# Optimization experiments

Measured on AMD Instinct MI355X. Metric: run time of the kernel, lower is better.

Reference implementation:

```python
import jax, jax.numpy as jnp
import numpy as np

N = 1024
X_DIM = 128
Y_DIM = 128
HIDDEN = 256


def setup_inputs() -> dict:
    key = jax.random.key(0)
    ks = jax.random.split(key, 6)
    x_samples = jax.random.normal(ks[0], (N, X_DIM), dtype=jnp.float32)
    y_samples = jax.random.normal(ks[1], (N, Y_DIM), dtype=jnp.float32)
    in_dim = X_DIM + Y_DIM
    # Linear params (kaiming-uniform-ish small init)
    W1 = jax.random.normal(ks[2], (in_dim, HIDDEN), dtype=jnp.float32) / np.sqrt(in_dim)
    b1 = jnp.zeros((HIDDEN,), dtype=jnp.float32)
    W2 = jax.random.normal(ks[3], (HIDDEN, 1), dtype=jnp.float32) / np.sqrt(HIDDEN)
    b2 = jnp.zeros((1,), dtype=jnp.float32)
    return {"x_samples": x_samples, "y_samples": y_samples,
            "W1": W1, "b1": b1, "W2": W2, "b2": b2}


def reference(x_samples, y_samples, W1, b1, W2, b2):
    n = y_samples.shape[0]
    W1x, W1y = W1[:X_DIM], W1[X_DIM:]
    xp = x_samples @ W1x          # [N, H]  (x_tile[i, j] = x[j])
    yp = y_samples @ W1y          # [N, H]  (y_tile[i, j] = y[i])
    # T0: F(cat([x_i, y_i])) on the diagonal pairs -> [N, 1]
    T0 = jax.nn.relu(xp + yp + b1) @ W2 + b2
    # T1: F over all pairs (i, j) -> [N, N, 1]
    h = jax.nn.relu(yp[:, None, :] + xp[None, :, :] + b1)   # [N, N, H]
    T1 = h @ W2 + b2                                        # [N, N, 1]
    lse = jax.scipy.special.logsumexp(T1, axis=1)           # [N, 1] over dim=1
    lower_bound = T0.mean() - (lse.mean() - jnp.log(jnp.float32(n)))
    return lower_bound
```

## Files before the change

### kernel.cpp

```cpp
#include <hip/hip_runtime.h>

#define N_SAMP 1024
#define XD     128
#define HID    256


__global__ __launch_bounds__(256) void gemm_xy(
    const float* __restrict__ x, const float* __restrict__ y,
    const float* __restrict__ W1, const float* __restrict__ b1,
    float* __restrict__ xpb, float* __restrict__ yp)
{
    const int k  = threadIdx.x;
    const int r0 = blockIdx.x * 4;

    float ax0 = 0.f, ax1 = 0.f, ax2 = 0.f, ax3 = 0.f;
    float ay0 = 0.f, ay1 = 0.f, ay2 = 0.f, ay3 = 0.f;

    #pragma unroll 4
    for (int d = 0; d < XD; ++d) {
        const float wx = W1[d * HID + k];
        const float wy = W1[(XD + d) * HID + k];
        ax0 = fmaf(x[(r0 + 0) * XD + d], wx, ax0);
        ax1 = fmaf(x[(r0 + 1) * XD + d], wx, ax1);
        ax2 = fmaf(x[(r0 + 2) * XD + d], wx, ax2);
        ax3 = fmaf(x[(r0 + 3) * XD + d], wx, ax3);
        ay0 = fmaf(y[(r0 + 0) * XD + d], wy, ay0);
        ay1 = fmaf(y[(r0 + 1) * XD + d], wy, ay1);
        ay2 = fmaf(y[(r0 + 2) * XD + d], wy, ay2);
        ay3 = fmaf(y[(r0 + 3) * XD + d], wy, ay3);
    }

    const float bk = b1[k];
    xpb[(r0 + 0) * HID + k] = ax0 + bk;
    xpb[(r0 + 1) * HID + k] = ax1 + bk;
    xpb[(r0 + 2) * HID + k] = ax2 + bk;
    xpb[(r0 + 3) * HID + k] = ax3 + bk;
    yp [(r0 + 0) * HID + k] = ay0;
    yp [(r0 + 1) * HID + k] = ay1;
    yp [(r0 + 2) * HID + k] = ay2;
    yp [(r0 + 3) * HID + k] = ay3;
}

__global__ __launch_bounds__(256) void pair_lse(
    const float* __restrict__ yp, const float* __restrict__ xpb,
    const float* __restrict__ W2,
    float* __restrict__ S, float* __restrict__ T0sum)
{
    const int STRIDE = 260;
    __shared__ float ys[16 * 260];
    __shared__ float xs[16 * 260];

    const int tid = threadIdx.x;
    const int bi  = blockIdx.y;
    const int bj  = blockIdx.x;

    for (int idx = tid * 4; idx < 16 * 256; idx += 1024) {
        const int r = idx >> 8, c = idx & 255;
        *(float4*)&ys[r * STRIDE + c] = *(const float4*)&yp [(bi * 16 + r) * HID + c];
        *(float4*)&xs[r * STRIDE + c] = *(const float4*)&xpb[(bj * 16 + r) * HID + c];
    }
    __syncthreads();

    const int ti = tid >> 4;
    const int tj = tid & 15;
    const float* yrow = &ys[ti * STRIDE];
    const float* xrow = &xs[tj * STRIDE];

    float acc = 0.f;
    #pragma unroll 8
    for (int c = 0; c < HID; c += 4) {
        const float4 a = *(const float4*)&yrow[c];
        const float4 b = *(const float4*)&xrow[c];
        const float4 w = *(const float4*)&W2[c];
        acc = fmaf(fmaxf(a.x + b.x, 0.f), w.x, acc);
        acc = fmaf(fmaxf(a.y + b.y, 0.f), w.y, acc);
        acc = fmaf(fmaxf(a.z + b.z, 0.f), w.z, acc);
        acc = fmaf(fmaxf(a.w + b.w, 0.f), w.w, acc);
    }

    float e = __expf(acc);
    #pragma unroll
    for (int off = 8; off; off >>= 1) e += __shfl_xor(e, off, 16);
    const int gi = bi * 16 + ti;
    if (tj == 0) atomicAdd(&S[gi], e);

    if (bi == bj) {
        float dv = (ti == tj) ? acc : 0.f;
        #pragma unroll
        for (int off = 32; off; off >>= 1) dv += __shfl_xor(dv, off, 64);
        if ((tid & 63) == 0) atomicAdd(T0sum, dv);
    }
}

__global__ __launch_bounds__(256) void finalize(
    const float* __restrict__ S, const float* __restrict__ T0sum,
    const float* __restrict__ b2, float* __restrict__ out)
{
    __shared__ float red[4];
    const int tid = threadIdx.x;

    float ls = 0.f;
    for (int i = tid; i < N_SAMP; i += 256) ls += logf(S[i]);
    #pragma unroll
    for (int off = 32; off; off >>= 1) ls += __shfl_xor(ls, off, 64);
    if ((tid & 63) == 0) red[tid >> 6] = ls;
    __syncthreads();

    if (tid == 0) {
        const float lse_sum = red[0] + red[1] + red[2] + red[3];
        const float t0_mean  = T0sum[0] / (float)N_SAMP + b2[0];
        const float lse_mean = lse_sum / (float)N_SAMP + b2[0] - logf((float)N_SAMP);
        out[0] = t0_mean - lse_mean;
    }
}

extern "C" void kernel_launch(void* const* d_in, const int* in_sizes, int n_in,
                              void* d_out, int out_size, void* d_ws, size_t ws_size,
                              hipStream_t stream)
{
    const float* x  = (const float*)d_in[0];
    const float* y  = (const float*)d_in[1];
    const float* W1 = (const float*)d_in[2];
    const float* b1 = (const float*)d_in[3];
    const float* W2 = (const float*)d_in[4];
    const float* b2 = (const float*)d_in[5];

    float* ws   = (float*)d_ws;
    float* S    = ws;
    float* T0s  = ws + 1024;
    float* xpb  = ws + 2048;
    float* yp   = ws + 2048 + N_SAMP * HID;

    hipMemsetAsync(d_ws, 0, (1024 + 1) * sizeof(float), stream);

    gemm_xy <<<dim3(N_SAMP / 4), dim3(256), 0, stream>>>(x, y, W1, b1, xpb, yp);
    pair_lse<<<dim3(64, 64),     dim3(256), 0, stream>>>(yp, xpb, W2, S, T0s);
    finalize<<<dim3(1),          dim3(256), 0, stream>>>(S, T0s, b2, (float*)d_out);
}
```

Measured before the change: 118.2 us.

## Register-tile pair_lse: 8 y-rows per wave with wave-uniform loads, 64 x-rows in LDS

Restructures the pairwise kernel so each thread computes 8 (i,j) pairs. The y rows are wave-uniform and read straight from global memory, which should turn them into scalar or broadcast loads, while a 64-row x tile is staged in LDS. This cuts the LDS reads per FMA and the number of blocks and atomics, and reuses each x element across 8 y rows. In exchange it uses more registers and has fewer blocks (512), which may limit occupancy, and the per-lane LDS row reads with stride 260 could hit bank conflicts.

Result: no change. 119.1 us (+0.7%).

```diff
diff --git a/kernel.cpp b/kernel.cpp
--- a/kernel.cpp
+++ b/kernel.cpp
@@ -41,54 +41,72 @@
     yp [(r0 + 3) * HID + k] = ay3;
 }
 
-__global__ __launch_bounds__(256) void pair_lse(
+#define XSTR 260
+__global__ __launch_bounds__(256, 2) void pair_lse(
     const float* __restrict__ yp, const float* __restrict__ xpb,
     const float* __restrict__ W2,
     float* __restrict__ S, float* __restrict__ T0sum)
 {
-    const int STRIDE = 260;
-    __shared__ float ys[16 * 260];
-    __shared__ float xs[16 * 260];
+    __shared__ float xs[64 * XSTR];
 
     const int tid = threadIdx.x;
+    const int bj  = blockIdx.x;
     const int bi  = blockIdx.y;
-    const int bj  = blockIdx.x;
 
-    for (int idx = tid * 4; idx < 16 * 256; idx += 1024) {
+    for (int idx = tid * 4; idx < 64 * 256; idx += 1024) {
         const int r = idx >> 8, c = idx & 255;
-        *(float4*)&ys[r * STRIDE + c] = *(const float4*)&yp [(bi * 16 + r) * HID + c];
-        *(float4*)&xs[r * STRIDE + c] = *(const float4*)&xpb[(bj * 16 + r) * HID + c];
+        *(float4*)&xs[r * XSTR + c] = *(const float4*)&xpb[(bj * 64 + r) * HID + c];
     }
     __syncthreads();
 
-    const int ti = tid >> 4;
-    const int tj = tid & 15;
-    const float* yrow = &ys[ti * STRIDE];
-    const float* xrow = &xs[tj * STRIDE];
+    const int wv   = __builtin_amdgcn_readfirstlane(tid >> 6);
+    const int lane = tid & 63;
+    const int i0   = bi * 32 + wv * 8;
+    const float* __restrict__ yb   = yp + i0 * HID;
+    const float* __restrict__ xrow = &xs[lane * XSTR];
 
-    float acc = 0.f;
-    #pragma unroll 8
+    float acc[8];
+    #pragma unroll
+    for (int ii = 0; ii < 8; ++ii) acc[ii] = 0.f;
+
+    #pragma unroll 2
     for (int c = 0; c < HID; c += 4) {
-        const float4 a = *(const float4*)&yrow[c];
-        const float4 b = *(const float4*)&xrow[c];
-        const float4 w = *(const float4*)&W2[c];
-        acc = fmaf(fmaxf(a.x + b.x, 0.f), w.x, acc);
-        acc = fmaf(fmaxf(a.y + b.y, 0.f), w.y, acc);
-        acc = fmaf(fmaxf(a.z + b.z, 0.f), w.z, acc);
-        acc = fmaf(fmaxf(a.w + b.w, 0.f), w.w, acc);
+        const float4 xv = *(const float4*)&xrow[c];
+        const float4 w  = *(const float4*)&W2[c];
+        float4 yv[8];
+        #pragma unroll
+        for (int ii = 0; ii < 8; ++ii)
+            yv[ii] = *(const float4*)&yb[ii * HID + c];
+        #pragma unroll
+        for (int ii = 0; ii < 8; ++ii) {
+            acc[ii] = fmaf(fmaxf(yv[ii].x + xv.x, 0.f), w.x, acc[ii]);
+            acc[ii] = fmaf(fmaxf(yv[ii].y + xv.y, 0.f), w.y, acc[ii]);
+            acc[ii] = fmaf(fmaxf(yv[ii].z + xv.z, 0.f), w.z, acc[ii]);
+            acc[ii] = fmaf(fmaxf(yv[ii].w + xv.w, 0.f), w.w, acc[ii]);
+        }
     }
 
-    float e = __expf(acc);
+    float ex[8];
     #pragma unroll
-    for (int off = 8; off; off >>= 1) e += __shfl_xor(e, off, 16);
-    const int gi = bi * 16 + ti;
-    if (tj == 0) atomicAdd(&S[gi], e);
+    for (int ii = 0; ii < 8; ++ii) {
+        float e = __expf(acc[ii]);
+        #pragma unroll
+        for (int off = 32; off; off >>= 1) e += __shfl_xor(e, off, 64);
+        ex[ii] = e;
+    }
+    if (lane == 0) {
+        #pragma unroll
+        for (int ii = 0; ii < 8; ++ii) atomicAdd(&S[i0 + ii], ex[ii]);
+    }
 
-    if (bi == bj) {
-        float dv = (ti == tj) ? acc : 0.f;
+    if (bj == (bi >> 1)) {
+        float dv = 0.f;
+        #pragma unroll
+        for (int ii = 0; ii < 8; ++ii)
+            if (i0 + ii - bj * 64 == lane) dv += acc[ii];
         #pragma unroll
         for (int off = 32; off; off >>= 1) dv += __shfl_xor(dv, off, 64);
-        if ((tid & 63) == 0) atomicAdd(T0sum, dv);
+        if (lane == 0) atomicAdd(T0sum, dv);
     }
 }
 
@@ -134,6 +152,6 @@
     hipMemsetAsync(d_ws, 0, (1024 + 1) * sizeof(float), stream);
 
     gemm_xy <<<dim3(N_SAMP / 4), dim3(256), 0, stream>>>(x, y, W1, b1, xpb, yp);
-    pair_lse<<<dim3(64, 64),     dim3(256), 0, stream>>>(yp, xpb, W2, S, T0s);
+    pair_lse<<<dim3(16, 32),     dim3(256), 0, stream>>>(yp, xpb, W2, S, T0s);
     finalize<<<dim3(1),          dim3(256), 0, stream>>>(S, T0s, b2, (float*)d_out);
 }
```

## Transpose projections to k-major and register-tile pair kernel 2x4 per thread

Applied to the files above, without the earlier changes.

The projection kernel now writes xp and yp transposed (hidden-major) so the pair kernel can read coalesced float4/float2 slices straight from global memory, with no shared-memory staging. Each thread computes a 2x4 block of pairs instead of one, which reuses the loaded values and cuts the grid from 4096 to 512 blocks and the number of atomics. The memset is folded into the first kernel, removing one launch. The trade-off is that every inner-loop operand now comes from global/L2 memory rather than LDS, and far fewer blocks are available to fill the GPU.

New measurement: 116.1 us. No clear change (-1.8%).

```diff
diff --git a/kernel.cpp b/kernel.cpp
--- a/kernel.cpp
+++ b/kernel.cpp
@@ -8,10 +8,14 @@
 __global__ __launch_bounds__(256) void gemm_xy(
     const float* __restrict__ x, const float* __restrict__ y,
     const float* __restrict__ W1, const float* __restrict__ b1,
-    float* __restrict__ xpb, float* __restrict__ yp)
+    float* __restrict__ xpbT, float* __restrict__ ypT,
+    float* __restrict__ S, float* __restrict__ T0sum)
 {
     const int k  = threadIdx.x;
     const int r0 = blockIdx.x * 4;
+
+    if (threadIdx.x < 4) S[blockIdx.x * 4 + threadIdx.x] = 0.f;
+    if (blockIdx.x == 0 && threadIdx.x == 4) T0sum[0] = 0.f;
 
     float ax0 = 0.f, ax1 = 0.f, ax2 = 0.f, ax3 = 0.f;
     float ay0 = 0.f, ay1 = 0.f, ay2 = 0.f, ay3 = 0.f;
@@ -31,61 +35,62 @@
     }
 
     const float bk = b1[k];
-    xpb[(r0 + 0) * HID + k] = ax0 + bk;
-    xpb[(r0 + 1) * HID + k] = ax1 + bk;
-    xpb[(r0 + 2) * HID + k] = ax2 + bk;
-    xpb[(r0 + 3) * HID + k] = ax3 + bk;
-    yp [(r0 + 0) * HID + k] = ay0;
-    yp [(r0 + 1) * HID + k] = ay1;
-    yp [(r0 + 2) * HID + k] = ay2;
-    yp [(r0 + 3) * HID + k] = ay3;
+    float4 xs = make_float4(ax0 + bk, ax1 + bk, ax2 + bk, ax3 + bk);
+    float4 ys = make_float4(ay0, ay1, ay2, ay3);
+    *(float4*)&xpbT[k * N_SAMP + r0] = xs;
+    *(float4*)&ypT [k * N_SAMP + r0] = ys;
 }
 
 __global__ __launch_bounds__(256) void pair_lse(
-    const float* __restrict__ yp, const float* __restrict__ xpb,
+    const float* __restrict__ ypT, const float* __restrict__ xpbT,
     const float* __restrict__ W2,
     float* __restrict__ S, float* __restrict__ T0sum)
 {
-    const int STRIDE = 260;
-    __shared__ float ys[16 * 260];
-    __shared__ float xs[16 * 260];
+    const int tid = threadIdx.x;
+    const int tj  = tid & 15;
+    const int ti  = tid >> 4;
+    const int bj  = blockIdx.x;
+    const int bi  = blockIdx.y;
+    const int j0  = bj * 64 + tj * 4;
+    const int i0  = bi * 32 + ti * 2;
 
-    const int tid = threadIdx.x;
-    const int bi  = blockIdx.y;
-    const int bj  = blockIdx.x;
+    float acc[2][4];
+    #pragma unroll
+    for (int a = 0; a < 2; ++a)
+        #pragma unroll
+        for (int b = 0; b < 4; ++b) acc[a][b] = 0.f;
 
-    for (int idx = tid * 4; idx < 16 * 256; idx += 1024) {
-        const int r = idx >> 8, c = idx & 255;
-        *(float4*)&ys[r * STRIDE + c] = *(const float4*)&yp [(bi * 16 + r) * HID + c];
-        *(float4*)&xs[r * STRIDE + c] = *(const float4*)&xpb[(bj * 16 + r) * HID + c];
-    }
-    __syncthreads();
-
-    const int ti = tid >> 4;
-    const int tj = tid & 15;
-    const float* yrow = &ys[ti * STRIDE];
-    const float* xrow = &xs[tj * STRIDE];
-
-    float acc = 0.f;
-    #pragma unroll 8
-    for (int c = 0; c < HID; c += 4) {
-        const float4 a = *(const float4*)&yrow[c];
-        const float4 b = *(const float4*)&xrow[c];
-        const float4 w = *(const float4*)&W2[c];
-        acc = fmaf(fmaxf(a.x + b.x, 0.f), w.x, acc);
-        acc = fmaf(fmaxf(a.y + b.y, 0.f), w.y, acc);
-        acc = fmaf(fmaxf(a.z + b.z, 0.f), w.z, acc);
-        acc = fmaf(fmaxf(a.w + b.w, 0.f), w.w, acc);
+    #pragma unroll 4
+    for (int k = 0; k < HID; ++k) {
+        const float4 xv = *(const float4*)&xpbT[k * N_SAMP + j0];
+        const float2 yv = *(const float2*)&ypT [k * N_SAMP + i0];
+        const float  w  = W2[k];
+        acc[0][0] = fmaf(fmaxf(yv.x + xv.x, 0.f), w, acc[0][0]);
+        acc[0][1] = fmaf(fmaxf(yv.x + xv.y, 0.f), w, acc[0][1]);
+        acc[0][2] = fmaf(fmaxf(yv.x + xv.z, 0.f), w, acc[0][2]);
+        acc[0][3] = fmaf(fmaxf(yv.x + xv.w, 0.f), w, acc[0][3]);
+        acc[1][0] = fmaf(fmaxf(yv.y + xv.x, 0.f), w, acc[1][0]);
+        acc[1][1] = fmaf(fmaxf(yv.y + xv.y, 0.f), w, acc[1][1]);
+        acc[1][2] = fmaf(fmaxf(yv.y + xv.z, 0.f), w, acc[1][2]);
+        acc[1][3] = fmaf(fmaxf(yv.y + xv.w, 0.f), w, acc[1][3]);
     }
 
-    float e = __expf(acc);
     #pragma unroll
-    for (int off = 8; off; off >>= 1) e += __shfl_xor(e, off, 16);
-    const int gi = bi * 16 + ti;
-    if (tj == 0) atomicAdd(&S[gi], e);
+    for (int a = 0; a < 2; ++a) {
+        float e = __expf(acc[a][0]) + __expf(acc[a][1])
+                + __expf(acc[a][2]) + __expf(acc[a][3]);
+        #pragma unroll
+        for (int off = 8; off; off >>= 1) e += __shfl_xor(e, off, 16);
+        if (tj == 0) atomicAdd(&S[i0 + a], e);
+    }
 
-    if (bi == bj) {
-        float dv = (ti == tj) ? acc : 0.f;
+    if (bj == (bi >> 1)) {
+        float dv = 0.f;
+        #pragma unroll
+        for (int a = 0; a < 2; ++a)
+            #pragma unroll
+            for (int b = 0; b < 4; ++b)
+                if (i0 + a == j0 + b) dv += acc[a][b];
         #pragma unroll
         for (int off = 32; off; off >>= 1) dv += __shfl_xor(dv, off, 64);
         if ((tid & 63) == 0) atomicAdd(T0sum, dv);
@@ -128,12 +133,11 @@
     float* ws   = (float*)d_ws;
     float* S    = ws;
     float* T0s  = ws + 1024;
-    float* xpb  = ws + 2048;
-    float* yp   = ws + 2048 + N_SAMP * HID;
+    float* xpbT = ws + 2048;
+    float* ypT  = ws + 2048 + HID * N_SAMP;
 
-    hipMemsetAsync(d_ws, 0, (1024 + 1) * sizeof(float), stream);
-
-    gemm_xy <<<dim3(N_SAMP / 4), dim3(256), 0, stream>>>(x, y, W1, b1, xpb, yp);
-    pair_lse<<<dim3(64, 64),     dim3(256), 0, stream>>>(yp, xpb, W2, S, T0s);
+    gemm_xy <<<dim3(N_SAMP / 4), dim3(256), 0, stream>>>(x, y, W1, b1,
+                                                         xpbT, ypT, S, T0s);
+    pair_lse<<<dim3(16, 32),     dim3(256), 0, stream>>>(ypT, xpbT, W2, S, T0s);
     finalize<<<dim3(1),          dim3(256), 0, stream>>>(S, T0s, b2, (float*)d_out);
 }
```
